# Kernel tuning notes

Hardware: AMD Instinct MI355X
Metric: run time of the kernel (lower is better)

## Reference

```python
import jax, jax.numpy as jnp
import numpy as np

B = 512          # batch
H = 1024         # lstm hidden size
L = 2            # lstm layers
T = 144          # max_length
INPUT_SIZE = 16  # activity vocab
OUTPUT_SIZE = 17 # acts logits (16) + duration (1)
COND = 32        # conditionals_size
COND_H = 512     # conditional_hidden_size
ENC = H - COND_H # encoding_size = 512
EMB = ENC - 1    # embedding dim (concat with duration scalar -> ENC)


def setup_inputs() -> dict:
    key = jax.random.key(0)
    ks = jax.random.split(key, 16)
    s = 0.02
    return {
        "batch_size": B,
        "h0": jax.random.normal(ks[0], (L, B, H), jnp.float32) * s,
        "c0": jax.random.normal(ks[1], (L, B, H), jnp.float32) * s,
        "conditionals": jax.random.normal(ks[2], (B, COND), jnp.float32),
        "target_acts": jax.random.randint(ks[3], (B, T), 0, INPUT_SIZE),
        "target_durs": jax.random.uniform(ks[4], (B, T), jnp.float32),
        "emb_table": jax.random.normal(ks[5], (INPUT_SIZE, EMB), jnp.float32) * s,
        "ff_W": jax.random.normal(ks[6], (COND_H, COND), jnp.float32) * s,
        "ff_b": jnp.zeros((COND_H,), jnp.float32),
        "Wih": jax.random.normal(ks[7], (L, 4 * H, H), jnp.float32) * s,
        "Whh": jax.random.normal(ks[8], (L, 4 * H, H), jnp.float32) * s,
        "bih": jnp.zeros((L, 4 * H), jnp.float32),
        "bhh": jnp.zeros((L, 4 * H), jnp.float32),
        "fc_W": jax.random.normal(ks[9], (OUTPUT_SIZE, H), jnp.float32) * s,
        "fc_b": jnp.zeros((OUTPUT_SIZE,), jnp.float32),
    }


def reference(batch_size, h0, c0, conditionals, target_acts, target_durs,
              emb_table, ff_W, ff_b, Wih, Whh, bih, bhh, fc_W, fc_b):
    # conditional projection, injected at every step input: [B, COND_H]
    cond_h = conditionals @ ff_W.T + ff_b

    # teacher forcing: step 0 sees SOS (act=0, dur=0); step j>=1 sees target[:, j-1]
    acts_in = jnp.concatenate(
        [jnp.zeros((B, 1), target_acts.dtype), target_acts[:, :-1]], axis=1).T  # [T, B]
    durs_in = jnp.concatenate(
        [jnp.zeros((B, 1), target_durs.dtype), target_durs[:, :-1]], axis=1).T  # [T, B]

    def step(carry, xin):
        h, c = carry                      # each [L, B, H]
        act, dur = xin                    # [B], [B]
        emb = emb_table[act]              # [B, EMB]
        # CustomDurationEmbeddingConcat: concat(embed(act), dur) -> ENC, then concat cond -> H
        x = jnp.concatenate([emb, dur[:, None], cond_h], axis=-1)  # [B, H]
        hs, cs = [], []
        for l in range(L):
            gates = x @ Wih[l].T + h[l] @ Whh[l].T + bih[l] + bhh[l]  # [B, 4H]
            i, f, g, o = jnp.split(gates, 4, axis=-1)  # PyTorch gate order i,f,g,o
            cl = jax.nn.sigmoid(f) * c[l] + jax.nn.sigmoid(i) * jnp.tanh(g)
            hl = jax.nn.sigmoid(o) * jnp.tanh(cl)
            hs.append(hl)
            cs.append(cl)
            x = hl
        pred = x @ fc_W.T + fc_b          # [B, OUTPUT_SIZE]
        return (jnp.stack(hs), jnp.stack(cs)), pred

    _, preds = jax.lax.scan(step, (h0, c0), (acts_in, durs_in))  # preds [T, B, OUT]
    out = preds.transpose(1, 0, 2)                               # [B, T, OUT]
    logits = out[..., : OUTPUT_SIZE - 1]
    dur = out[..., OUTPUT_SIZE - 1:]
    # log-softmax over activity logits; log(sigmoid(dur)) for durations
    return jnp.concatenate(
        [jax.nn.log_softmax(logits, axis=-1), jax.nn.log_sigmoid(dur)], axis=-1)
```

## Files before the change

### kernel.cpp

```cpp
#include <hip/hip_runtime.h>
#include <hip/hip_bf16.h>
#include <stdint.h>

#define B_   512
#define H_   1024
#define T_   144
#define NG   4096
#define NOUT 17

typedef __bf16 bf16_t;
typedef __bf16 bf16x8 __attribute__((ext_vector_type(8)));
typedef float  f32x4  __attribute__((ext_vector_type(4)));

__device__ __host__ __forceinline__ int npack(int n) {
  int g = n >> 10, j = n & 1023;
  return ((j >> 4) << 6) + (g << 4) + (j & 15);
}
__device__ __forceinline__ float sigf(float x) { return 1.f / (1.f + __expf(-x)); }
__device__ __forceinline__ float tanhf_(float x) { return 1.f - 2.f / (__expf(2.f * x) + 1.f); }


__global__ void k_pack_wA(const float* __restrict__ Whh0, bf16_t* __restrict__ PB1) {
  int idx = blockIdx.x * 256 + threadIdx.x;
  int n = idx >> 7, kc = idx & 127;
  const float* s = Whh0 + (size_t)n * H_ + kc * 8;
  bf16x8 v;
#pragma unroll
  for (int e = 0; e < 8; ++e) v[e] = (bf16_t)s[e];
  int np = npack(n), jt = np >> 7, row = np & 127;
  *(bf16x8*)(PB1 + (size_t)jt * 131072 + (kc >> 2) * 4096 + row * 32 + (kc & 3) * 8) = v;
}

__global__ void k_pack_wB(const float* __restrict__ Wih1, const float* __restrict__ Whh1,
                          bf16_t* __restrict__ PB2) {
  int idx = blockIdx.x * 256 + threadIdx.x;
  int n = idx >> 8, kc = idx & 255;
  int k = kc * 8;
  const float* s = (k < H_) ? (Wih1 + (size_t)n * H_ + k) : (Whh1 + (size_t)n * H_ + (k - H_));
  bf16x8 v;
#pragma unroll
  for (int e = 0; e < 8; ++e) v[e] = (bf16_t)s[e];
  int np = npack(n), jt = np >> 7, row = np & 127;
  *(bf16x8*)(PB2 + (size_t)jt * 262144 + (kc >> 2) * 4096 + row * 32 + (kc & 3) * 8) = v;
}

__global__ void k_G(const float* __restrict__ Wih0, const float* __restrict__ ffW,
                    const float* __restrict__ ffb, float* __restrict__ G) {
  int n = blockIdx.x * 256 + threadIdx.x;
  float acc[33];
#pragma unroll
  for (int c = 0; c < 33; ++c) acc[c] = 0.f;
  for (int k = 0; k < 512; ++k) {
    float wv = Wih0[(size_t)n * H_ + 512 + k];
    const float* fr = ffW + (size_t)k * 32;
#pragma unroll
    for (int c = 0; c < 32; ++c) acc[c] += wv * fr[c];
    acc[32] += wv * ffb[k];
  }
  for (int c = 0; c < 33; ++c) G[(size_t)c * NG + n] = acc[c];
}

__global__ void k_CHp(const float* __restrict__ cond, const float* __restrict__ G,
                      const float* __restrict__ bih0, const float* __restrict__ bhh0,
                      float* __restrict__ CHp) {
  int idx = blockIdx.x * 256 + threadIdx.x;
  int b = idx >> 12, n = idx & 4095;
  float acc = bih0[n] + bhh0[n] + G[(size_t)32 * NG + n];
  const float* cb = cond + (size_t)b * 32;
#pragma unroll
  for (int c = 0; c < 32; ++c) acc += cb[c] * G[(size_t)c * NG + n];
  CHp[(size_t)b * NG + npack(n)] = acc;
}

__global__ void k_E16(const float* __restrict__ emb, const float* __restrict__ Wih0,
                      float* __restrict__ E16p) {
  int idx = blockIdx.x * 256 + threadIdx.x;
  int a = idx & 15, n = idx >> 4;
  const float* er = emb + (size_t)a * 511;
  const float* wr = Wih0 + (size_t)n * H_;
  float acc = 0.f;
  for (int k = 0; k < 511; ++k) acc += er[k] * wr[k];
  E16p[(size_t)a * NG + npack(n)] = acc;
}

__global__ void k_misc(const float* __restrict__ Wih0, const float* __restrict__ bih,
                       const float* __restrict__ bhh, const float* __restrict__ fcW,
                       bf16_t* __restrict__ fcWp, float* __restrict__ biasBp,
                       float* __restrict__ wcolp) {
  int idx = blockIdx.x * 256 + threadIdx.x;
  if (idx < NG) {
    int np = npack(idx);
    biasBp[np] = bih[NG + idx] + bhh[NG + idx];
    wcolp[np]  = Wih0[(size_t)idx * H_ + 511];
  }
  if (idx < 17 * H_) fcWp[idx] = (bf16_t)fcW[idx];
}

__global__ void k_init(const float* __restrict__ h0,
                       bf16_t* __restrict__ pah0i, bf16_t* __restrict__ pah1a) {
  int idx = blockIdx.x * 256 + threadIdx.x;
  int b = idx >> 7, kc = idx & 127;
  const float* s0 = h0 + (size_t)b * H_ + kc * 8;
  const float* s1 = s0 + (size_t)B_ * H_;
  bf16x8 v0, v1;
#pragma unroll
  for (int e = 0; e < 8; ++e) { v0[e] = (bf16_t)s0[e]; v1[e] = (bf16_t)s1[e]; }
  size_t po = (size_t)(kc >> 2) * 16384 + b * 32 + (kc & 3) * 8;
  *(bf16x8*)(pah0i + po) = v0;
  *(bf16x8*)(pah1a + po) = v1;
}

__global__ void k_out(const float* __restrict__ preds, const float* __restrict__ fcb,
                      float* __restrict__ out) {
  int idx = blockIdx.x * 256 + threadIdx.x;
  if (idx >= T_ * B_) return;
  int t = idx % T_, b = idx / T_;
  const float* pr = preds + ((size_t)t * B_ + b) * NOUT;
  float v[NOUT];
#pragma unroll
  for (int o = 0; o < NOUT; ++o) v[o] = pr[o] + fcb[o];
  float m = v[0];
#pragma unroll
  for (int o = 1; o < 16; ++o) m = fmaxf(m, v[o]);
  float s = 0.f;
#pragma unroll
  for (int o = 0; o < 16; ++o) s += expf(v[o] - m);
  float lse = m + logf(s);
  float* dst = out + ((size_t)b * T_ + t) * NOUT;
#pragma unroll
  for (int o = 0; o < 16; ++o) dst[o] = v[o] - lse;
  float x = v[16];
  dst[16] = (x > 0.f) ? -log1pf(expf(-x)) : (x - log1pf(expf(x)));
}


struct Params {
  const int* acts; const float* durs;
  const bf16_t* PB1; const bf16_t* PB2;
  const float* CHp; const float* E16p; const float* wcolp; const float* biasBp;
  const bf16_t* fcW;
  const float* c0in;
  const bf16_t* pah0i;
  bf16_t* pah0a; bf16_t* pah0b; bf16_t* pah1a; bf16_t* pah1b;
  unsigned* slots; float* preds;
};

__device__ __forceinline__ void gbar(unsigned* slots, unsigned phase, int tid, int wg) {
  __syncthreads();
  if (tid == 0) {
    __builtin_amdgcn_fence(__ATOMIC_RELEASE, "agent");
    __hip_atomic_store(slots + (size_t)wg * 16, phase, __ATOMIC_RELAXED, __HIP_MEMORY_SCOPE_AGENT);
  }
  {
    const unsigned* a0 = slots + (size_t)tid * 16;
    while (__hip_atomic_load(a0, __ATOMIC_RELAXED, __HIP_MEMORY_SCOPE_SYSTEM) < phase)
      __builtin_amdgcn_s_sleep(1);
  }
  __syncthreads();
}

struct AF { bf16x8 a, e; };
struct B6 { bf16x8 v0, v1, v2, v3, v4, v5; };
struct PS { bf16x8 a, b0, b1, b2, b3, c0, c1, c2, c3; };

#define VMW(N) { asm volatile("s_waitcnt vmcnt(" #N ")" ::: "memory"); \
                 __builtin_amdgcn_sched_barrier(0); }
#define LGK0   { asm volatile("s_waitcnt lgkmcnt(0)" ::: "memory"); \
                 __builtin_amdgcn_sched_barrier(0); }
#define WGBAR  { __builtin_amdgcn_s_barrier(); __builtin_amdgcn_sched_barrier(0); }

#define MFM(ACC, AV, BV) ACC = __builtin_amdgcn_mfma_f32_16x16x32_bf16(AV, BV, ACC, 0, 0, 0)

__device__ __forceinline__ void ldF2(AF& f, const char* pa, const char* pe) {
  asm volatile("global_load_dwordx4 %0, %2, off sc1\n\t"
               "global_load_dwordx4 %1, %3, off sc1"
               : "=&v"(f.a), "=&v"(f.e) : "v"(pa), "v"(pe));
}

__device__ __forceinline__ void ldB6(B6& r, const char* b1k, const char* b2k, const char* b2k32) {
  asm volatile("global_load_dwordx4 %0, %2, off\n\t"
               "global_load_dwordx4 %1, %3, off"
               : "=&v"(r.v0), "=&v"(r.v1) : "v"(b1k), "v"(b1k + 4096));
  asm volatile("global_load_dwordx4 %0, %2, off\n\t"
               "global_load_dwordx4 %1, %3, off"
               : "=&v"(r.v2), "=&v"(r.v3) : "v"(b2k), "v"(b2k + 4096));
  asm volatile("global_load_dwordx4 %0, %2, off\n\t"
               "global_load_dwordx4 %1, %3, off"
               : "=&v"(r.v4), "=&v"(r.v5) : "v"(b2k32), "v"(b2k32 + 4096));
}

__device__ __forceinline__ void dswr(char* lb, int tid, const B6& r) {
  *(bf16x8*)(lb + tid * 16)         = r.v0;
  *(bf16x8*)(lb + 4096 + tid * 16)  = r.v1;
  *(bf16x8*)(lb + 8192 + tid * 16)  = r.v2;
  *(bf16x8*)(lb + 12288 + tid * 16) = r.v3;
  *(bf16x8*)(lb + 16384 + tid * 16) = r.v4;
  *(bf16x8*)(lb + 20480 + tid * 16) = r.v5;
}

__device__ __forceinline__ void cmpM(f32x4 (&a0)[2][4], f32x4 (&a1)[2][4],
                                     const char* lbR, const AF& f) {
#pragma unroll
  for (int s = 0; s < 2; ++s)
#pragma unroll
    for (int g = 0; g < 4; ++g) {
      bf16x8 w0 = *(const bf16x8*)(lbR + s * 4096 + g * 1024);
      MFM(a0[s][g], f.a, w0);
    }
#pragma unroll
  for (int s = 0; s < 2; ++s)
#pragma unroll
    for (int g = 0; g < 4; ++g) {
      bf16x8 wi = *(const bf16x8*)(lbR + 8192 + s * 4096 + g * 1024);
      MFM(a1[s][g], f.a, wi);
      bf16x8 wh = *(const bf16x8*)(lbR + 16384 + s * 4096 + g * 1024);
      MFM(a1[s][g], f.e, wh);
    }
}

__global__ __launch_bounds__(256, 1) void lstm_main(Params p) {
  __shared__ __align__(16) char smem[3 * 24576];

  const int tid = threadIdx.x;
  const int w = tid >> 6, l = tid & 63;
  const int wg = blockIdx.x;
  const int mt2 = wg >> 5;
  const int jt  = ((wg >> 3) & 3) * 8 + (wg & 7);
  const int jj = l & 15, rq = l >> 4;
  const int a_off = (mt2 * 64 + w * 16 + jj) * 64 + rq * 16;
  const char* B1 = (const char*)p.PB1 + (size_t)jt * 262144;
  const char* B2 = (const char*)p.PB2 + (size_t)jt * 524288;
  const int heb = jt * 16384 + jj;
  const int frag_base = jj * 64 + rq * 16;

  bf16x8 fcw[2][2], fw16[2][2];
#pragma unroll
  for (int s = 0; s < 2; ++s) {
    const char* fwp = (const char*)p.fcW;
    fcw[s][0]  = *(const bf16x8*)(fwp + jj * 2048 + (jt * 2 + s) * 32);
    fcw[s][1]  = *(const bf16x8*)(fwp + jj * 2048 + (jt * 2 + s) * 32 + 16);
    fw16[s][0] = *(const bf16x8*)(fwp + 16 * 2048 + (jt * 2 + s) * 32);
    fw16[s][1] = *(const bf16x8*)(fwp + 16 * 2048 + (jt * 2 + s) * 32 + 16);
  }

  float chv[2][4][4], cv0[2][4], cv1[2][4], bzv[2][4], wcv[2][4];
#pragma unroll
  for (int s = 0; s < 2; ++s) {
    int npb = (jt * 2 + s) * 64;
#pragma unroll
    for (int qq = 0; qq < 4; ++qq) {
      int b = mt2 * 64 + w * 16 + rq * 4 + qq;
      int jcol = (jt * 2 + s) * 16 + jj;
      cv0[s][qq] = p.c0in[(size_t)b * H_ + jcol];
      cv1[s][qq] = p.c0in[(size_t)B_ * H_ + (size_t)b * H_ + jcol];
#pragma unroll
      for (int g = 0; g < 4; ++g)
        chv[s][qq][g] = p.CHp[(size_t)b * NG + npb + g * 16 + jj];
    }
#pragma unroll
    for (int g = 0; g < 4; ++g) {
      bzv[s][g] = p.biasBp[npb + g * 16 + jj];
      wcv[s][g] = p.wcolp[npb + g * 16 + jj];
    }
  }
  VMW(0);

  unsigned phase = 0;

  {
    f32x4 acc0[2][4];
#pragma unroll
    for (int s = 0; s < 2; ++s)
#pragma unroll
      for (int g = 0; g < 4; ++g) acc0[s][g] = (f32x4){0.f, 0.f, 0.f, 0.f};

    const char* Ai = (const char*)p.pah0i;
    PS S0, S1, S2;
    auto Pp = [&](int kk, PS& S) {
      asm volatile("global_load_dwordx4 %0, %1, off"
                   : "=&v"(S.a) : "v"(Ai + (size_t)kk * 32768 + a_off));
      const char* p0 = B1 + (size_t)kk * 8192 + frag_base;
      asm volatile("global_load_dwordx4 %0, %4, off\n\t"
                   "global_load_dwordx4 %1, %4, off offset:1024\n\t"
                   "global_load_dwordx4 %2, %4, off offset:2048\n\t"
                   "global_load_dwordx4 %3, %4, off offset:3072"
                   : "=&v"(S.b0), "=&v"(S.b1), "=&v"(S.b2), "=&v"(S.b3) : "v"(p0));
      const char* p1 = p0 + 4096;
      asm volatile("global_load_dwordx4 %0, %4, off\n\t"
                   "global_load_dwordx4 %1, %4, off offset:1024\n\t"
                   "global_load_dwordx4 %2, %4, off offset:2048\n\t"
                   "global_load_dwordx4 %3, %4, off offset:3072"
                   : "=&v"(S.c0), "=&v"(S.c1), "=&v"(S.c2), "=&v"(S.c3) : "v"(p1));
    };
    auto Cp = [&](const PS& S) {
      MFM(acc0[0][0], S.a, S.b0); MFM(acc0[0][1], S.a, S.b1);
      MFM(acc0[0][2], S.a, S.b2); MFM(acc0[0][3], S.a, S.b3);
      MFM(acc0[1][0], S.a, S.c0); MFM(acc0[1][1], S.a, S.c1);
      MFM(acc0[1][2], S.a, S.c2); MFM(acc0[1][3], S.a, S.c3);
    };
    Pp(0, S0); Pp(1, S1);
#pragma unroll 1
    for (int o = 0; o < 10; ++o) {
      Pp(3 * o + 2, S2); VMW(18); Cp(S0);
      Pp(3 * o + 3, S0); VMW(18); Cp(S1);
      Pp(3 * o + 4, S1); VMW(18); Cp(S2);
    }
    VMW(9); Cp(S0);
    VMW(0); Cp(S1);

    bf16_t* H0n = p.pah0a;
#pragma unroll
    for (int s = 0; s < 2; ++s)
#pragma unroll
      for (int qq = 0; qq < 4; ++qq) {
        int b = mt2 * 64 + w * 16 + rq * 4 + qq;
        int npb = (jt * 2 + s) * 64;
        float pre[4];
#pragma unroll
        for (int g = 0; g < 4; ++g)
          pre[g] = acc0[s][g][qq] + chv[s][qq][g] + p.E16p[npb + g * 16 + jj];
        float cn = sigf(pre[1]) * cv0[s][qq] + sigf(pre[0]) * tanhf_(pre[2]);
        float hn = sigf(pre[3]) * tanhf_(cn);
        cv0[s][qq] = cn;
        H0n[(size_t)heb + s * 16 + b * 32] = (bf16_t)hn;
      }
    ++phase; gbar(p.slots, phase, tid, wg);
  }

#pragma unroll 1
  for (int t = 0; t < T_; ++t) {
    const char* Ah0 = (const char*)((t & 1) ? p.pah0b : p.pah0a);
    bf16_t*     H0n = (t & 1) ? p.pah0a : p.pah0b;
    const char* Ah1 = (const char*)((t & 1) ? p.pah1b : p.pah1a);
    bf16_t*     H1n = (t & 1) ? p.pah1a : p.pah1b;

    f32x4 acc0[2][4], acc1[2][4];
#pragma unroll
    for (int s = 0; s < 2; ++s)
#pragma unroll
      for (int g = 0; g < 4; ++g) {
        acc0[s][g] = (f32x4){0.f, 0.f, 0.f, 0.f};
        acc1[s][g] = (f32x4){0.f, 0.f, 0.f, 0.f};
      }

    B6 Br0, Br1;
    AF F0, F1;
    auto LB = [&](B6& r, int kk) {
      ldB6(r, B1 + (size_t)kk * 8192 + tid * 16,
              B2 + (size_t)kk * 8192 + tid * 16,
              B2 + (size_t)(kk + 32) * 8192 + tid * 16);
    };
    auto LA = [&](AF& f, int kk) {
      ldF2(f, Ah0 + (size_t)kk * 32768 + a_off, Ah1 + (size_t)kk * 32768 + a_off);
    };

    LB(Br0, 0); LB(Br1, 1); LA(F0, 0); LA(F1, 1);
    VMW(10);
    dswr(smem, tid, Br0);
    LB(Br0, 2);
    int bufR = 0;

#pragma unroll 1
    for (int kk = 0; kk < 28; kk += 2) {
      {
        int bw = bufR + 1; if (bw == 3) bw = 0;
        VMW(8);
        dswr(smem + bw * 24576, tid, Br1);
        LB(Br1, kk + 3);
        LGK0; WGBAR;
        cmpM(acc0, acc1, smem + bufR * 24576 + frag_base, F0);
        LA(F0, kk + 2);
        bufR = bw;
      }
      {
        int bw = bufR + 1; if (bw == 3) bw = 0;
        VMW(8);
        dswr(smem + bw * 24576, tid, Br0);
        LB(Br0, kk + 4);
        LGK0; WGBAR;
        cmpM(acc0, acc1, smem + bufR * 24576 + frag_base, F1);
        LA(F1, kk + 3);
        bufR = bw;
      }
    }
    {
      int bw = bufR + 1; if (bw == 3) bw = 0;
      VMW(8);
      dswr(smem + bw * 24576, tid, Br1);
      LB(Br1, 31);
      LGK0; WGBAR;
      cmpM(acc0, acc1, smem + bufR * 24576 + frag_base, F0);
      LA(F0, 30);
      bufR = bw;
    }
    {
      int bw = bufR + 1; if (bw == 3) bw = 0;
      VMW(8);
      dswr(smem + bw * 24576, tid, Br0);
      LGK0; WGBAR;
      cmpM(acc0, acc1, smem + bufR * 24576 + frag_base, F1);
      LA(F1, 31);
      bufR = bw;
    }
    {
      int bw = bufR + 1; if (bw == 3) bw = 0;
      VMW(2);
      dswr(smem + bw * 24576, tid, Br1);
      LGK0; WGBAR;
      cmpM(acc0, acc1, smem + bufR * 24576 + frag_base, F0);
      bufR = bw;
    }
    {
      VMW(0);
      cmpM(acc0, acc1, smem + bufR * 24576 + frag_base, F1);
    }

#pragma unroll
    for (int qq = 0; qq < 4; ++qq) {
      int b = mt2 * 64 + w * 16 + rq * 4 + qq;
      int act = p.acts[(size_t)b * T_ + t];
      float dur = p.durs[(size_t)b * T_ + t];
      float hn1v[2];
#pragma unroll
      for (int s = 0; s < 2; ++s) {
        int npb = (jt * 2 + s) * 64;
        float pre1[4];
#pragma unroll
        for (int g = 0; g < 4; ++g) pre1[g] = acc1[s][g][qq] + bzv[s][g];
        float cn1 = sigf(pre1[1]) * cv1[s][qq] + sigf(pre1[0]) * tanhf_(pre1[2]);
        float hn1 = sigf(pre1[3]) * tanhf_(cn1);
        cv1[s][qq] = cn1;
        H1n[(size_t)heb + s * 16 + b * 32] = (bf16_t)hn1;
        hn1v[s] = hn1;
        float pre0[4];
#pragma unroll
        for (int g = 0; g < 4; ++g)
          pre0[g] = acc0[s][g][qq] + chv[s][qq][g]
                  + p.E16p[(size_t)act * NG + npb + g * 16 + jj] + dur * wcv[s][g];
        float cn0 = sigf(pre0[1]) * cv0[s][qq] + sigf(pre0[0]) * tanhf_(pre0[2]);
        float hn0 = sigf(pre0[3]) * tanhf_(cn0);
        cv0[s][qq] = cn0;
        H0n[(size_t)heb + s * 16 + b * 32] = (bf16_t)hn0;
      }
      float accO = 0.f, acc16 = 0.f;
      int base = l & 48;
#pragma unroll
      for (int s = 0; s < 2; ++s) {
#pragma unroll
        for (int sc = 0; sc < 8; ++sc) {
          float hs = __shfl(hn1v[s], base | sc, 64);
          accO  += hs * (float)fcw[s][0][sc];
          acc16 += hs * (float)fw16[s][0][sc];
        }
#pragma unroll
        for (int sc = 0; sc < 8; ++sc) {
          float hs = __shfl(hn1v[s], base | (8 + sc), 64);
          accO  += hs * (float)fcw[s][1][sc];
          acc16 += hs * (float)fw16[s][1][sc];
        }
      }
      float* pb = p.preds + ((size_t)t * B_ + b) * NOUT;
      atomicAdd(pb + jj, accO);
      if (jj == 15) atomicAdd(pb + 16, acc16);
    }
    ++phase; gbar(p.slots, phase, tid, wg);
  }
}


extern "C" void kernel_launch(void* const* d_in, const int* in_sizes, int n_in,
                              void* d_out, int out_size, void* d_ws, size_t ws_size,
                              hipStream_t stream) {
  (void)in_sizes; (void)n_in; (void)out_size; (void)ws_size;
  const float* h0   = (const float*)d_in[1];
  const float* c0   = (const float*)d_in[2];
  const float* cond = (const float*)d_in[3];
  const int*   acts = (const int*)d_in[4];
  const float* durs = (const float*)d_in[5];
  const float* emb  = (const float*)d_in[6];
  const float* ffW  = (const float*)d_in[7];
  const float* ffb  = (const float*)d_in[8];
  const float* Wih  = (const float*)d_in[9];
  const float* Whh  = (const float*)d_in[10];
  const float* bih  = (const float*)d_in[11];
  const float* bhh  = (const float*)d_in[12];
  const float* fcW  = (const float*)d_in[13];
  const float* fcb  = (const float*)d_in[14];

  char* ws = (char*)d_ws;
  size_t off = 0;
  auto alloc = [&](size_t bytes) -> char* {
    char* p0 = ws + off;
    off = (off + bytes + 255) & ~(size_t)255;
    return p0;
  };
  unsigned* slots = (unsigned*)alloc(256 * 64);
  bf16_t* PB1     = (bf16_t*)alloc((size_t)NG * H_ * 2);
  bf16_t* PB2     = (bf16_t*)alloc((size_t)NG * 2048 * 2);
  float*  CHp     = (float*)alloc((size_t)B_ * NG * 4);
  float*  E16p    = (float*)alloc((size_t)16 * NG * 4);
  float*  wcolp   = (float*)alloc((size_t)NG * 4);
  float*  biasBp  = (float*)alloc((size_t)NG * 4);
  float*  G       = (float*)alloc((size_t)33 * NG * 4);
  bf16_t* fcWp    = (bf16_t*)alloc((size_t)17 * H_ * 2);
  bf16_t* pah0i   = (bf16_t*)alloc((size_t)B_ * H_ * 2);
  bf16_t* pah0a   = (bf16_t*)alloc((size_t)B_ * H_ * 2);
  bf16_t* pah0b   = (bf16_t*)alloc((size_t)B_ * H_ * 2);
  bf16_t* pah1a   = (bf16_t*)alloc((size_t)B_ * H_ * 2);
  bf16_t* pah1b   = (bf16_t*)alloc((size_t)B_ * H_ * 2);
  float*  preds   = (float*)alloc((size_t)T_ * B_ * NOUT * 4);

  hipMemsetAsync(slots, 0, 256 * 64, stream);
  hipMemsetAsync(preds, 0, (size_t)T_ * B_ * NOUT * 4, stream);
  k_pack_wA<<<2048, 256, 0, stream>>>(Whh, PB1);
  k_pack_wB<<<4096, 256, 0, stream>>>(Wih + (size_t)NG * H_, Whh + (size_t)NG * H_, PB2);
  k_G<<<16, 256, 0, stream>>>(Wih, ffW, ffb, G);
  k_CHp<<<8192, 256, 0, stream>>>(cond, G, bih, bhh, CHp);
  k_E16<<<256, 256, 0, stream>>>(emb, Wih, E16p);
  k_misc<<<68, 256, 0, stream>>>(Wih, bih, bhh, fcW, fcWp, biasBp, wcolp);
  k_init<<<256, 256, 0, stream>>>(h0, pah0i, pah1a);

  Params prm;
  prm.acts = acts; prm.durs = durs;
  prm.PB1 = PB1; prm.PB2 = PB2;
  prm.CHp = CHp; prm.E16p = E16p; prm.wcolp = wcolp; prm.biasBp = biasBp;
  prm.fcW = fcWp;
  prm.c0in = c0;
  prm.pah0i = pah0i;
  prm.pah0a = pah0a; prm.pah0b = pah0b; prm.pah1a = pah1a; prm.pah1b = pah1b;
  prm.slots = slots; prm.preds = preds;

  lstm_main<<<dim3(256), dim3(256), 0, stream>>>(prm);
  k_out<<<(T_ * B_ + 255) / 256, 256, 0, stream>>>(preds, fcb, (float*)d_out);
}
```

Measured before the change: 6.489 ms.

## Stage activations in LDS and keep weights in registers per wave

The per-step GEMM is re-tiled. Each wave now owns a 32-row by 16-column sub-tile and loads its weight fragments straight from global memory into registers. The hidden-state activations are staged through a swizzled, triple-buffered LDS tile, where before the weights went through LDS. This shrinks LDS traffic and footprint, since the activation tile is smaller than the weight tile, and reuses each weight fragment across two MFMA row blocks. In exchange, register pressure rises, vmcnt accounting gets more complex, and the output projection now issues more shuffles and atomics per wave.

```diff
diff --git a/kernel.cpp b/kernel.cpp
--- a/kernel.cpp
+++ b/kernel.cpp
@@ -159,9 +159,8 @@
   __syncthreads();
 }
 
-struct AF { bf16x8 a, e; };
-struct B6 { bf16x8 v0, v1, v2, v3, v4, v5; };
-struct PS { bf16x8 a, b0, b1, b2, b3, c0, c1, c2, c3; };
+struct BS { bf16x8 b[4], c[4], d[4]; };
+struct PS { bf16x8 a0, a1, b0, b1, b2, b3; };
 
 #define VMW(N) { asm volatile("s_waitcnt vmcnt(" #N ")" ::: "memory"); \
                  __builtin_amdgcn_sched_barrier(0); }
@@ -171,55 +170,16 @@
 
 #define MFM(ACC, AV, BV) ACC = __builtin_amdgcn_mfma_f32_16x16x32_bf16(AV, BV, ACC, 0, 0, 0)
 
-__device__ __forceinline__ void ldF2(AF& f, const char* pa, const char* pe) {
-  asm volatile("global_load_dwordx4 %0, %2, off sc1\n\t"
-               "global_load_dwordx4 %1, %3, off sc1"
-               : "=&v"(f.a), "=&v"(f.e) : "v"(pa), "v"(pe));
-}
-
-__device__ __forceinline__ void ldB6(B6& r, const char* b1k, const char* b2k, const char* b2k32) {
-  asm volatile("global_load_dwordx4 %0, %2, off\n\t"
-               "global_load_dwordx4 %1, %3, off"
-               : "=&v"(r.v0), "=&v"(r.v1) : "v"(b1k), "v"(b1k + 4096));
-  asm volatile("global_load_dwordx4 %0, %2, off\n\t"
-               "global_load_dwordx4 %1, %3, off"
-               : "=&v"(r.v2), "=&v"(r.v3) : "v"(b2k), "v"(b2k + 4096));
-  asm volatile("global_load_dwordx4 %0, %2, off\n\t"
-               "global_load_dwordx4 %1, %3, off"
-               : "=&v"(r.v4), "=&v"(r.v5) : "v"(b2k32), "v"(b2k32 + 4096));
-}
-
-__device__ __forceinline__ void dswr(char* lb, int tid, const B6& r) {
-  *(bf16x8*)(lb + tid * 16)         = r.v0;
-  *(bf16x8*)(lb + 4096 + tid * 16)  = r.v1;
-  *(bf16x8*)(lb + 8192 + tid * 16)  = r.v2;
-  *(bf16x8*)(lb + 12288 + tid * 16) = r.v3;
-  *(bf16x8*)(lb + 16384 + tid * 16) = r.v4;
-  *(bf16x8*)(lb + 20480 + tid * 16) = r.v5;
-}
-
-__device__ __forceinline__ void cmpM(f32x4 (&a0)[2][4], f32x4 (&a1)[2][4],
-                                     const char* lbR, const AF& f) {
-#pragma unroll
-  for (int s = 0; s < 2; ++s)
-#pragma unroll
-    for (int g = 0; g < 4; ++g) {
-      bf16x8 w0 = *(const bf16x8*)(lbR + s * 4096 + g * 1024);
-      MFM(a0[s][g], f.a, w0);
-    }
-#pragma unroll
-  for (int s = 0; s < 2; ++s)
-#pragma unroll
-    for (int g = 0; g < 4; ++g) {
-      bf16x8 wi = *(const bf16x8*)(lbR + 8192 + s * 4096 + g * 1024);
-      MFM(a1[s][g], f.a, wi);
-      bf16x8 wh = *(const bf16x8*)(lbR + 16384 + s * 4096 + g * 1024);
-      MFM(a1[s][g], f.e, wh);
-    }
+__device__ __forceinline__ void ldB4(bf16x8* r, const char* p) {
+  asm volatile("global_load_dwordx4 %0, %4, off\n\t"
+               "global_load_dwordx4 %1, %4, off offset:1024\n\t"
+               "global_load_dwordx4 %2, %4, off offset:2048\n\t"
+               "global_load_dwordx4 %3, %4, off offset:3072"
+               : "=&v"(r[0]), "=&v"(r[1]), "=&v"(r[2]), "=&v"(r[3]) : "v"(p));
 }
 
 __global__ __launch_bounds__(256, 1) void lstm_main(Params p) {
-  __shared__ __align__(16) char smem[3 * 24576];
+  __shared__ __align__(16) char smem[3 * 8192];
 
   const int tid = threadIdx.x;
   const int w = tid >> 6, l = tid & 63;
@@ -227,102 +187,109 @@
   const int mt2 = wg >> 5;
   const int jt  = ((wg >> 3) & 3) * 8 + (wg & 7);
   const int jj = l & 15, rq = l >> 4;
-  const int a_off = (mt2 * 64 + w * 16 + jj) * 64 + rq * 16;
+  const int mh = w >> 1;
+  const int st = w & 1;
+  const int bfrag = st * 4096 + jj * 64 + rq * 16;
   const char* B1 = (const char*)p.PB1 + (size_t)jt * 262144;
   const char* B2 = (const char*)p.PB2 + (size_t)jt * 524288;
-  const int heb = jt * 16384 + jj;
-  const int frag_base = jj * 64 + rq * 16;
-
-  bf16x8 fcw[2][2], fw16[2][2];
-#pragma unroll
-  for (int s = 0; s < 2; ++s) {
+  const int heb = jt * 16384 + st * 16 + jj;
+  const int npb = (jt * 2 + st) * 64;
+
+  const int sh    = tid >> 7;
+  const int srow  = tid & 63;
+  const int shalf = (tid >> 6) & 1;
+  const int g_aoff = (mt2 * 64 + srow) * 64 + shalf * 32;
+  const int lwr = srow * 128;
+  const int ws0 = ((sh * 4 + shalf * 2 + 0) ^ (srow & 7)) * 16;
+  const int ws1 = ((sh * 4 + shalf * 2 + 1) ^ (srow & 7)) * 16;
+  const int r00 = (mh * 32 + jj) * 128 + (((0 + rq) ^ (jj & 7)) * 16);
+  const int r01 = (mh * 32 + jj) * 128 + (((4 + rq) ^ (jj & 7)) * 16);
+  const int r10 = r00 + 2048;
+  const int r11 = r01 + 2048;
+
+  bf16x8 fcw_a, fcw_b, fw16_a, fw16_b;
+  {
     const char* fwp = (const char*)p.fcW;
-    fcw[s][0]  = *(const bf16x8*)(fwp + jj * 2048 + (jt * 2 + s) * 32);
-    fcw[s][1]  = *(const bf16x8*)(fwp + jj * 2048 + (jt * 2 + s) * 32 + 16);
-    fw16[s][0] = *(const bf16x8*)(fwp + 16 * 2048 + (jt * 2 + s) * 32);
-    fw16[s][1] = *(const bf16x8*)(fwp + 16 * 2048 + (jt * 2 + s) * 32 + 16);
-  }
-
-  float chv[2][4][4], cv0[2][4], cv1[2][4], bzv[2][4], wcv[2][4];
-#pragma unroll
-  for (int s = 0; s < 2; ++s) {
-    int npb = (jt * 2 + s) * 64;
+    fcw_a  = *(const bf16x8*)(fwp + jj * 2048 + (jt * 2 + st) * 32);
+    fcw_b  = *(const bf16x8*)(fwp + jj * 2048 + (jt * 2 + st) * 32 + 16);
+    fw16_a = *(const bf16x8*)(fwp + 16 * 2048 + (jt * 2 + st) * 32);
+    fw16_b = *(const bf16x8*)(fwp + 16 * 2048 + (jt * 2 + st) * 32 + 16);
+  }
+
+  float chv[2][4][4], cv0[2][4], cv1[2][4], bzv[4], wcv[4];
+#pragma unroll
+  for (int m = 0; m < 2; ++m)
 #pragma unroll
     for (int qq = 0; qq < 4; ++qq) {
-      int b = mt2 * 64 + w * 16 + rq * 4 + qq;
-      int jcol = (jt * 2 + s) * 16 + jj;
-      cv0[s][qq] = p.c0in[(size_t)b * H_ + jcol];
-      cv1[s][qq] = p.c0in[(size_t)B_ * H_ + (size_t)b * H_ + jcol];
+      int b = mt2 * 64 + mh * 32 + m * 16 + rq * 4 + qq;
+      int jcol = (jt * 2 + st) * 16 + jj;
+      cv0[m][qq] = p.c0in[(size_t)b * H_ + jcol];
+      cv1[m][qq] = p.c0in[(size_t)B_ * H_ + (size_t)b * H_ + jcol];
 #pragma unroll
       for (int g = 0; g < 4; ++g)
-        chv[s][qq][g] = p.CHp[(size_t)b * NG + npb + g * 16 + jj];
-    }
-#pragma unroll
-    for (int g = 0; g < 4; ++g) {
-      bzv[s][g] = p.biasBp[npb + g * 16 + jj];
-      wcv[s][g] = p.wcolp[npb + g * 16 + jj];
-    }
+        chv[m][qq][g] = p.CHp[(size_t)b * NG + npb + g * 16 + jj];
+    }
+#pragma unroll
+  for (int g = 0; g < 4; ++g) {
+    bzv[g] = p.biasBp[npb + g * 16 + jj];
+    wcv[g] = p.wcolp[npb + g * 16 + jj];
   }
   VMW(0);
 
   unsigned phase = 0;
 
   {
-    f32x4 acc0[2][4];
-#pragma unroll
-    for (int s = 0; s < 2; ++s)
-#pragma unroll
-      for (int g = 0; g < 4; ++g) acc0[s][g] = (f32x4){0.f, 0.f, 0.f, 0.f};
+    f32x4 accp[4][2];
+#pragma unroll
+    for (int g = 0; g < 4; ++g)
+#pragma unroll
+      for (int m = 0; m < 2; ++m) accp[g][m] = (f32x4){0.f, 0.f, 0.f, 0.f};
 
     const char* Ai = (const char*)p.pah0i;
+    const int pa_off = (mt2 * 64 + mh * 32 + jj) * 64 + rq * 16;
     PS S0, S1, S2;
     auto Pp = [&](int kk, PS& S) {
-      asm volatile("global_load_dwordx4 %0, %1, off"
-                   : "=&v"(S.a) : "v"(Ai + (size_t)kk * 32768 + a_off));
-      const char* p0 = B1 + (size_t)kk * 8192 + frag_base;
+      const char* pa = Ai + (size_t)kk * 32768 + pa_off;
+      asm volatile("global_load_dwordx4 %0, %2, off\n\t"
+                   "global_load_dwordx4 %1, %2, off offset:1024"
+                   : "=&v"(S.a0), "=&v"(S.a1) : "v"(pa));
+      const char* p0 = B1 + (size_t)kk * 8192 + bfrag;
       asm volatile("global_load_dwordx4 %0, %4, off\n\t"
                    "global_load_dwordx4 %1, %4, off offset:1024\n\t"
                    "global_load_dwordx4 %2, %4, off offset:2048\n\t"
                    "global_load_dwordx4 %3, %4, off offset:3072"
                    : "=&v"(S.b0), "=&v"(S.b1), "=&v"(S.b2), "=&v"(S.b3) : "v"(p0));
-      const char* p1 = p0 + 4096;
-      asm volatile("global_load_dwordx4 %0, %4, off\n\t"
-                   "global_load_dwordx4 %1, %4, off offset:1024\n\t"
-                   "global_load_dwordx4 %2, %4, off offset:2048\n\t"
-                   "global_load_dwordx4 %3, %4, off offset:3072"
-                   : "=&v"(S.c0), "=&v"(S.c1), "=&v"(S.c2), "=&v"(S.c3) : "v"(p1));
     };
     auto Cp = [&](const PS& S) {
-      MFM(acc0[0][0], S.a, S.b0); MFM(acc0[0][1], S.a, S.b1);
-      MFM(acc0[0][2], S.a, S.b2); MFM(acc0[0][3], S.a, S.b3);
-      MFM(acc0[1][0], S.a, S.c0); MFM(acc0[1][1], S.a, S.c1);
-      MFM(acc0[1][2], S.a, S.c2); MFM(acc0[1][3], S.a, S.c3);
+      MFM(accp[0][0], S.a0, S.b0); MFM(accp[0][1], S.a1, S.b0);
+      MFM(accp[1][0], S.a0, S.b1); MFM(accp[1][1], S.a1, S.b1);
+      MFM(accp[2][0], S.a0, S.b2); MFM(accp[2][1], S.a1, S.b2);
+      MFM(accp[3][0], S.a0, S.b3); MFM(accp[3][1], S.a1, S.b3);
     };
     Pp(0, S0); Pp(1, S1);
 #pragma unroll 1
     for (int o = 0; o < 10; ++o) {
-      Pp(3 * o + 2, S2); VMW(18); Cp(S0);
-      Pp(3 * o + 3, S0); VMW(18); Cp(S1);
-      Pp(3 * o + 4, S1); VMW(18); Cp(S2);
-    }
-    VMW(9); Cp(S0);
+      Pp(3 * o + 2, S2); VMW(12); Cp(S0);
+      Pp(3 * o + 3, S0); VMW(12); Cp(S1);
+      Pp(3 * o + 4, S1); VMW(12); Cp(S2);
+    }
+    VMW(6); Cp(S0);
     VMW(0); Cp(S1);
 
     bf16_t* H0n = p.pah0a;
 #pragma unroll
-    for (int s = 0; s < 2; ++s)
+    for (int m = 0; m < 2; ++m)
 #pragma unroll
       for (int qq = 0; qq < 4; ++qq) {
-        int b = mt2 * 64 + w * 16 + rq * 4 + qq;
-        int npb = (jt * 2 + s) * 64;
+        int b = mt2 * 64 + mh * 32 + m * 16 + rq * 4 + qq;
         float pre[4];
 #pragma unroll
         for (int g = 0; g < 4; ++g)
-          pre[g] = acc0[s][g][qq] + chv[s][qq][g] + p.E16p[npb + g * 16 + jj];
-        float cn = sigf(pre[1]) * cv0[s][qq] + sigf(pre[0]) * tanhf_(pre[2]);
+          pre[g] = accp[g][m][qq] + chv[m][qq][g] + p.E16p[npb + g * 16 + jj];
+        float cn = sigf(pre[1]) * cv0[m][qq] + sigf(pre[0]) * tanhf_(pre[2]);
         float hn = sigf(pre[3]) * tanhf_(cn);
-        cv0[s][qq] = cn;
-        H0n[(size_t)heb + s * 16 + b * 32] = (bf16_t)hn;
+        cv0[m][qq] = cn;
+        H0n[(size_t)heb + b * 32] = (bf16_t)hn;
       }
     ++phase; gbar(p.slots, phase, tid, wg);
   }
@@ -333,136 +300,184 @@
     bf16_t*     H0n = (t & 1) ? p.pah0a : p.pah0b;
     const char* Ah1 = (const char*)((t & 1) ? p.pah1b : p.pah1a);
     bf16_t*     H1n = (t & 1) ? p.pah1a : p.pah1b;
-
-    f32x4 acc0[2][4], acc1[2][4];
-#pragma unroll
-    for (int s = 0; s < 2; ++s)
-#pragma unroll
-      for (int g = 0; g < 4; ++g) {
-        acc0[s][g] = (f32x4){0.f, 0.f, 0.f, 0.f};
-        acc1[s][g] = (f32x4){0.f, 0.f, 0.f, 0.f};
+    const char* Asrc = sh ? Ah1 : Ah0;
+
+    f32x4 acc0[4][2], acc1[4][2];
+#pragma unroll
+    for (int g = 0; g < 4; ++g)
+#pragma unroll
+      for (int m = 0; m < 2; ++m) {
+        acc0[g][m] = (f32x4){0.f, 0.f, 0.f, 0.f};
+        acc1[g][m] = (f32x4){0.f, 0.f, 0.f, 0.f};
       }
 
-    B6 Br0, Br1;
-    AF F0, F1;
-    auto LB = [&](B6& r, int kk) {
-      ldB6(r, B1 + (size_t)kk * 8192 + tid * 16,
-              B2 + (size_t)kk * 8192 + tid * 16,
-              B2 + (size_t)(kk + 32) * 8192 + tid * 16);
-    };
-    auto LA = [&](AF& f, int kk) {
-      ldF2(f, Ah0 + (size_t)kk * 32768 + a_off, Ah1 + (size_t)kk * 32768 + a_off);
-    };
-
-    LB(Br0, 0); LB(Br1, 1); LA(F0, 0); LA(F1, 1);
-    VMW(10);
-    dswr(smem, tid, Br0);
-    LB(Br0, 2);
+    bf16x8 Ar0a, Ar0b, Ar1a, Ar1b;
+    BS Bs0, Bs1;
+    auto AST0 = [&](int kk) {
+      const char* s = Asrc + (size_t)kk * 32768 + g_aoff;
+      asm volatile("global_load_dwordx4 %0, %2, off sc1\n\t"
+                   "global_load_dwordx4 %1, %2, off offset:16 sc1"
+                   : "=&v"(Ar0a), "=&v"(Ar0b) : "v"(s));
+    };
+    auto AST1 = [&](int kk) {
+      const char* s = Asrc + (size_t)kk * 32768 + g_aoff;
+      asm volatile("global_load_dwordx4 %0, %2, off sc1\n\t"
+                   "global_load_dwordx4 %1, %2, off offset:16 sc1"
+                   : "=&v"(Ar1a), "=&v"(Ar1b) : "v"(s));
+    };
+    auto DSW0 = [&](char* buf) {
+      *(bf16x8*)(buf + lwr + ws0) = Ar0a;
+      *(bf16x8*)(buf + lwr + ws1) = Ar0b;
+    };
+    auto DSW1 = [&](char* buf) {
+      *(bf16x8*)(buf + lwr + ws0) = Ar1a;
+      *(bf16x8*)(buf + lwr + ws1) = Ar1b;
+    };
+    auto LBD0 = [&](int kk) {
+      ldB4(Bs0.b, B1 + (size_t)kk * 8192 + bfrag);
+      ldB4(Bs0.c, B2 + (size_t)kk * 8192 + bfrag);
+      ldB4(Bs0.d, B2 + (size_t)(kk + 32) * 8192 + bfrag);
+    };
+    auto LBD1 = [&](int kk) {
+      ldB4(Bs1.b, B1 + (size_t)kk * 8192 + bfrag);
+      ldB4(Bs1.c, B2 + (size_t)kk * 8192 + bfrag);
+      ldB4(Bs1.d, B2 + (size_t)(kk + 32) * 8192 + bfrag);
+    };
+    auto CMP0 = [&](const char* buf) {
+      bf16x8 a0 = *(const bf16x8*)(buf + r00);
+      bf16x8 a1 = *(const bf16x8*)(buf + r10);
+      bf16x8 e0 = *(const bf16x8*)(buf + r01);
+      bf16x8 e1 = *(const bf16x8*)(buf + r11);
+      LGK0;
+#pragma unroll
+      for (int g = 0; g < 4; ++g) { MFM(acc0[g][0], a0, Bs0.b[g]); MFM(acc0[g][1], a1, Bs0.b[g]); }
+#pragma unroll
+      for (int g = 0; g < 4; ++g) { MFM(acc1[g][0], a0, Bs0.c[g]); MFM(acc1[g][1], a1, Bs0.c[g]); }
+#pragma unroll
+      for (int g = 0; g < 4; ++g) { MFM(acc1[g][0], e0, Bs0.d[g]); MFM(acc1[g][1], e1, Bs0.d[g]); }
+    };
+    auto CMP1 = [&](const char* buf) {
+      bf16x8 a0 = *(const bf16x8*)(buf + r00);
+      bf16x8 a1 = *(const bf16x8*)(buf + r10);
+      bf16x8 e0 = *(const bf16x8*)(buf + r01);
+      bf16x8 e1 = *(const bf16x8*)(buf + r11);
+      LGK0;
+#pragma unroll
+      for (int g = 0; g < 4; ++g) { MFM(acc0[g][0], a0, Bs1.b[g]); MFM(acc0[g][1], a1, Bs1.b[g]); }
+#pragma unroll
+      for (int g = 0; g < 4; ++g) { MFM(acc1[g][0], a0, Bs1.c[g]); MFM(acc1[g][1], a1, Bs1.c[g]); }
+#pragma unroll
+      for (int g = 0; g < 4; ++g) { MFM(acc1[g][0], e0, Bs1.d[g]); MFM(acc1[g][1], e1, Bs1.d[g]); }
+    };
+
+    AST0(0); AST1(1); LBD0(0);
+    VMW(14);
+    DSW0(smem);
+    AST0(2); LBD1(1);
+    LGK0; WGBAR;
     int bufR = 0;
 
 #pragma unroll 1
     for (int kk = 0; kk < 28; kk += 2) {
       {
         int bw = bufR + 1; if (bw == 3) bw = 0;
-        VMW(8);
-        dswr(smem + bw * 24576, tid, Br1);
-        LB(Br1, kk + 3);
+        VMW(26);
+        DSW1(smem + bw * 8192);
+        AST1(kk + 3);
         LGK0; WGBAR;
-        cmpM(acc0, acc1, smem + bufR * 24576 + frag_base, F0);
-        LA(F0, kk + 2);
+        VMW(16);
+        CMP0(smem + bufR * 8192);
+        LBD0(kk + 2);
         bufR = bw;
       }
       {
         int bw = bufR + 1; if (bw == 3) bw = 0;
-        VMW(8);
-        dswr(smem + bw * 24576, tid, Br0);
-        LB(Br0, kk + 4);
+        VMW(26);
+        DSW0(smem + bw * 8192);
+        AST0(kk + 4);
         LGK0; WGBAR;
-        cmpM(acc0, acc1, smem + bufR * 24576 + frag_base, F1);
-        LA(F1, kk + 3);
+        VMW(16);
+        CMP1(smem + bufR * 8192);
+        LBD1(kk + 3);
         bufR = bw;
       }
     }
     {
       int bw = bufR + 1; if (bw == 3) bw = 0;
-      VMW(8);
-      dswr(smem + bw * 24576, tid, Br1);
-      LB(Br1, 31);
+      VMW(26);
+      DSW1(smem + bw * 8192);
+      AST1(31);
       LGK0; WGBAR;
-      cmpM(acc0, acc1, smem + bufR * 24576 + frag_base, F0);
-      LA(F0, 30);
+      VMW(16);
+      CMP0(smem + bufR * 8192);
+      LBD0(30);
       bufR = bw;
     }
     {
       int bw = bufR + 1; if (bw == 3) bw = 0;
-      VMW(8);
-      dswr(smem + bw * 24576, tid, Br0);
+      VMW(26);
+      DSW0(smem + bw * 8192);
       LGK0; WGBAR;
-      cmpM(acc0, acc1, smem + bufR * 24576 + frag_base, F1);
-      LA(F1, 31);
+      VMW(14);
+      CMP1(smem + bufR * 8192);
+      LBD1(31);
       bufR = bw;
     }
     {
       int bw = bufR + 1; if (bw == 3) bw = 0;
-      VMW(2);
-      dswr(smem + bw * 24576, tid, Br1);
+      VMW(24);
+      DSW1(smem + bw * 8192);
       LGK0; WGBAR;
-      cmpM(acc0, acc1, smem + bufR * 24576 + frag_base, F0);
+      VMW(12);
+      CMP0(smem + bufR * 8192);
       bufR = bw;
     }
     {
       VMW(0);
-      cmpM(acc0, acc1, smem + bufR * 24576 + frag_base, F1);
-    }
-
-#pragma unroll
-    for (int qq = 0; qq < 4; ++qq) {
-      int b = mt2 * 64 + w * 16 + rq * 4 + qq;
-      int act = p.acts[(size_t)b * T_ + t];
-      float dur = p.durs[(size_t)b * T_ + t];
-      float hn1v[2];
-#pragma unroll
-      for (int s = 0; s < 2; ++s) {
-        int npb = (jt * 2 + s) * 64;
+      CMP1(smem + bufR * 8192);
+    }
+
+#pragma unroll
+    for (int m = 0; m < 2; ++m)
+#pragma unroll
+      for (int qq = 0; qq < 4; ++qq) {
+        int b = mt2 * 64 + mh * 32 + m * 16 + rq * 4 + qq;
+        int act = p.acts[(size_t)b * T_ + t];
+        float dur = p.durs[(size_t)b * T_ + t];
         float pre1[4];
 #pragma unroll
-        for (int g = 0; g < 4; ++g) pre1[g] = acc1[s][g][qq] + bzv[s][g];
-        float cn1 = sigf(pre1[1]) * cv1[s][qq] + sigf(pre1[0]) * tanhf_(pre1[2]);
+        for (int g = 0; g < 4; ++g) pre1[g] = acc1[g][m][qq] + bzv[g];
+        float cn1 = sigf(pre1[1]) * cv1[m][qq] + sigf(pre1[0]) * tanhf_(pre1[2]);
         float hn1 = sigf(pre1[3]) * tanhf_(cn1);
-        cv1[s][qq] = cn1;
-        H1n[(size_t)heb + s * 16 + b * 32] = (bf16_t)hn1;
-        hn1v[s] = hn1;
+        cv1[m][qq] = cn1;
+        H1n[(size_t)heb + b * 32] = (bf16_t)hn1;
         float pre0[4];
 #pragma unroll
         for (int g = 0; g < 4; ++g)
-          pre0[g] = acc0[s][g][qq] + chv[s][qq][g]
-                  + p.E16p[(size_t)act * NG + npb + g * 16 + jj] + dur * wcv[s][g];
-        float cn0 = sigf(pre0[1]) * cv0[s][qq] + sigf(pre0[0]) * tanhf_(pre0[2]);
+          pre0[g] = acc0[g][m][qq] + chv[m][qq][g]
+                  + p.E16p[(size_t)act * NG + npb + g * 16 + jj] + dur * wcv[g];
+        float cn0 = sigf(pre0[1]) * cv0[m][qq] + sigf(pre0[0]) * tanhf_(pre0[2]);
         float hn0 = sigf(pre0[3]) * tanhf_(cn0);
-        cv0[s][qq] = cn0;
-        H0n[(size_t)heb + s * 16 + b * 32] = (bf16_t)hn0;
+        cv0[m][qq] = cn0;
+        H0n[(size_t)heb + b * 32] = (bf16_t)hn0;
+        float accO = 0.f, acc16 = 0.f;
+        int base = l & 48;
+#pragma unroll
+        for (int sc = 0; sc < 8; ++sc) {
+          float hs = __shfl(hn1, base | sc, 64);
+          accO  += hs * (float)fcw_a[sc];
+          acc16 += hs * (float)fw16_a[sc];
+        }
+#pragma unroll
+        for (int sc = 0; sc < 8; ++sc) {
+          float hs = __shfl(hn1, base | (8 + sc), 64);
+          accO  += hs * (float)fcw_b[sc];
+          acc16 += hs * (float)fw16_b[sc];
+        }
+        float* pb = p.preds + ((size_t)t * B_ + b) * NOUT;
+        atomicAdd(pb + jj, accO);
+        if (jj == 15) atomicAdd(pb + 16, acc16);
       }
-      float accO = 0.f, acc16 = 0.f;
-      int base = l & 48;
-#pragma unroll
-      for (int s = 0; s < 2; ++s) {
-#pragma unroll
-        for (int sc = 0; sc < 8; ++sc) {
-          float hs = __shfl(hn1v[s], base | sc, 64);
-          accO  += hs * (float)fcw[s][0][sc];
-          acc16 += hs * (float)fw16[s][0][sc];
-        }
-#pragma unroll
-        for (int sc = 0; sc < 8; ++sc) {
-          float hs = __shfl(hn1v[s], base | (8 + sc), 64);
-          accO  += hs * (float)fcw[s][1][sc];
-          acc16 += hs * (float)fw16[s][1][sc];
-        }
-      }
-      float* pb = p.preds + ((size_t)t * B_ + b) * NOUT;
-      atomicAdd(pb + jj, accO);
-      if (jj == 15) atomicAdd(pb + 16, acc16);
-    }
     ++phase; gbar(p.slots, phase, tid, wg);
   }
 }
```

New measurement: 7.008 ms. 8.0% more time.
